# Kernel optimization log

Hardware: AMD Instinct MI355X
Metric: run time of the kernel (lower is better)

Reference implementation:

```python
import jax, jax.numpy as jnp
import numpy as np


def setup_inputs() -> dict:
    key = jax.random.key(0)
    k1, k2 = jax.random.split(key)
    B, L, D = 8, 4096, 64
    x = jax.random.normal(k1, (B, L, D), dtype=jnp.float32)
    # per-token validity mask [B, L, 1] with 0/1 entries (outer product builds the pairwise mask)
    mask = jax.random.randint(k2, (B, L, 1), 0, 2, dtype=jnp.int32)
    return {"x": x, "mask": mask}


def reference(x, mask):
    # OriAttention with head=1: q = k = v = x, shapes [B, L, D]
    B, L, D = x.shape
    scale = D ** 0.25  # note: fourth root of d, as in the original
    scores = jnp.einsum('bqd,bkd->bqk', x, x) / scale  # [B, L, L]
    # pairwise mask via outer product of the [B, L, 1] token mask, then bool cast
    mf = mask.astype(jnp.float32)
    pair = jnp.matmul(mf, mf.transpose(0, 2, 1)) != 0.0  # [B, L, L] bool
    scores = jnp.where(pair, scores, jnp.float32(-10000000.0))
    # original softmaxes along dim=2 of [B, H, Lq, Lk], i.e. over the QUERY axis
    attn = jax.nn.softmax(scores, axis=1)  # normalize over q for each k
    # then transposes (2,3) and matmuls with v: out[b,k,:] = sum_q attn[b,q,k] * v[b,q,:]
    out = jnp.einsum('bqk,bqd->bkd', attn, x)  # [B, L, D]
    return out
```

## Files before the change

### kernel.cpp

```cpp
#include <hip/hip_runtime.h>
#include <stdint.h>

typedef __attribute__((ext_vector_type(8))) __bf16 bf16x8;
typedef __attribute__((ext_vector_type(4))) __bf16 bf16x4;
typedef __attribute__((ext_vector_type(4))) float f32x4;

#define MFMA_BF16(A, B, C) __builtin_amdgcn_mfma_f32_16x16x32_bf16((A), (B), (C), 0, 0, 0)
#define VBAR() asm volatile("s_waitcnt vmcnt(0) lgkmcnt(0)\ns_barrier" ::: "memory")

__device__ __forceinline__ void gload16(const void* g, void* l) {
  __builtin_amdgcn_global_load_lds((const __attribute__((address_space(1))) void*)g,
                                   (__attribute__((address_space(3))) void*)l, 16, 0, 0);
}

namespace {

constexpr int kBatch = 8;
constexpr int kL = 4096;
constexpr int kD = 64;
constexpr int kQB = 128;
constexpr int kKB = 64;
constexpr int kSlotPad = 4096;
constexpr int kMaxTiles = 64;
constexpr int kSlotCap = 2304;
constexpr int kSplits = 8;
constexpr float kC = 1.4426950408889634f / 2.8284271247461903f;

constexpr size_t kWsPartialOff = 0;
constexpr size_t kWsCountOff = 65536;
constexpr size_t kWsRankOff = 131136;
constexpr size_t kWsPlOff = 196672;
constexpr size_t kWsXchOff = 1376320;
constexpr size_t kWsVtgOff = 5570624;
constexpr size_t kWsPaccOff = 9764928;

__device__ __forceinline__ int fk(int r) { return (r & 3) | ((r >> 1) & 4); }

__device__ __forceinline__ size_t slotrow(int s, int b, int slot, bool fb) {
  return fb ? ((size_t)b * kL + slot) : ((size_t)(s * kBatch + b) * kSlotCap + slot);
}

__global__ __launch_bounds__(256) void k_prep(const float* __restrict__ x,
                                              const int* __restrict__ mask,
                                              float* __restrict__ partial,
                                              uint16_t* __restrict__ rank,
                                              int* __restrict__ counts,
                                              __bf16* __restrict__ xch,
                                              __bf16* __restrict__ vtg) {
  const int b = blockIdx.y;
  const int bx = blockIdx.x;
  const int t = threadIdx.x;

  if (bx >= 64) {
    const int part = bx - 64;
    __shared__ float sm[256];
    const int d = t & 63, rs = t >> 6;
    const float* xb = x + (size_t)b * kL * kD;
    float s = 0.0f;
    const int r0 = part * 128 + rs;
    for (int i = 0; i < 32; ++i) s += xb[(size_t)(r0 + i * 4) * kD + d];
    sm[t] = s;
    __syncthreads();
    if (t < 64)
      partial[(b * 32 + part) * 64 + t] = sm[t] + sm[t + 64] + sm[t + 128] + sm[t + 192];
    return;
  }

  __shared__ int scan[256];
  __shared__ int slotTab[64];
  __shared__ __align__(16) __bf16 tmp[kKB][80];

  const int* mb = mask + b * kL;
  const int r0 = t * 16;
  int msk16 = 0, cnt = 0;
#pragma unroll
  for (int i = 0; i < 16; ++i) {
    if (mb[r0 + i] != 0) { msk16 |= 1 << i; ++cnt; }
  }
  scan[t] = cnt;
  if (t < 64) slotTab[t] = -1;
  __syncthreads();
#pragma unroll
  for (int off = 1; off < 256; off <<= 1) {
    const int v = (t >= off) ? scan[t - off] : 0;
    __syncthreads();
    scan[t] += v;
    __syncthreads();
  }
  const int count = scan[255];
  const int base = bx * 64;
  {
    int rk = scan[t] - cnt;
#pragma unroll
    for (int i = 0; i < 16; ++i) {
      if (msk16 & (1 << i)) {
        if (rk >= base && rk < base + 64) slotTab[rk - base] = r0 + i;
        ++rk;
      }
    }
  }
  if (bx == 0) {
    int rk = scan[t] - cnt;
#pragma unroll
    for (int i = 0; i < 16; ++i) {
      if (msk16 & (1 << i)) { rank[b * kL + r0 + i] = (uint16_t)rk; ++rk; }
    }
    if (t == 0) counts[b] = count;
  }
  __syncthreads();

  const int NT = (count + kKB - 1) >> 6;
  if (bx >= NT) return;

  const int srow = t >> 2, q3 = t & 3;
  const int slot = base + srow;
  const int rowi = slotTab[srow];
  float v16[16];
  if (rowi >= 0) {
    const float4* p = (const float4*)(x + ((size_t)b * kL + rowi) * kD + q3 * 16);
    const float4 a0 = p[0], a1 = p[1], a2 = p[2], a3 = p[3];
    v16[0] = a0.x; v16[1] = a0.y; v16[2] = a0.z; v16[3] = a0.w;
    v16[4] = a1.x; v16[5] = a1.y; v16[6] = a1.z; v16[7] = a1.w;
    v16[8] = a2.x; v16[9] = a2.y; v16[10] = a2.z; v16[11] = a2.w;
    v16[12] = a3.x; v16[13] = a3.y; v16[14] = a3.z; v16[15] = a3.w;
  } else {
#pragma unroll
    for (int i = 0; i < 16; ++i) v16[i] = 0.0f;
  }
  bf16x8 u0, u1;
#pragma unroll
  for (int j = 0; j < 8; ++j) { u0[j] = (__bf16)v16[j]; u1[j] = (__bf16)v16[8 + j]; }

  {
    __bf16* xrow = xch + ((size_t)b * kSlotPad + slot) * kD;
    const int f = fk(srow);
    *(bf16x8*)(xrow + (((2 * q3) ^ f) << 3)) = u0;
    *(bf16x8*)(xrow + (((2 * q3 + 1) ^ f) << 3)) = u1;
  }
  *(bf16x8*)&tmp[srow][q3 * 16] = u0;
  *(bf16x8*)&tmp[srow][q3 * 16 + 8] = u1;
  __syncthreads();
  {
    const int d = t >> 2, kq = t & 3;
    bf16x8 c0, c1;
#pragma unroll
    for (int i = 0; i < 8; ++i) {
      c0[i] = tmp[kq * 16 + i][d];
      c1[i] = tmp[kq * 16 + 8 + i][d];
    }
    __bf16* vrow = vtg + (((size_t)b * kMaxTiles + bx) * kKB + d) * kD;
    const int e = d & 7;
    *(bf16x8*)(vrow + (((2 * kq) ^ e) << 3)) = c0;
    *(bf16x8*)(vrow + (((2 * kq + 1) ^ e) << 3)) = c1;
  }
}

__global__ __launch_bounds__(256, 4) void k_attn(const __bf16* __restrict__ xch,
                                                 const __bf16* __restrict__ vtg,
                                                 const int* __restrict__ counts,
                                                 float* __restrict__ pl,
                                                 __bf16* __restrict__ pacc) {
  const int b = blockIdx.x;
  const int s = blockIdx.y;
  const int qt = blockIdx.z;

  int cmax = 0;
#pragma unroll
  for (int i = 0; i < kBatch; ++i) cmax = max(cmax, counts[i]);
  const bool fb = cmax > kSlotCap;
  const int nS = fb ? 1 : (int)gridDim.y;
  if (fb && s > 0) return;

  const int count = counts[b];
  if (qt * kQB >= count) return;
  const int NTtot = (count + kKB - 1) >> 6;
  const int TPS = (NTtot + nS - 1) / nS;
  const int t0 = s * TPS;
  const int t1 = min(NTtot, t0 + TPS);

  const int tid = threadIdx.x;
  const int wave = tid >> 6;
  const int lane = tid & 63;
  const int lg = lane >> 4;
  const int lr = lane & 15;

  int qpos[2];
  bool qvalid[2];
  size_t sr[2];
#pragma unroll
  for (int h = 0; h < 2; ++h) {
    qpos[h] = qt * kQB + h * 64 + wave * 16 + lr;
    qvalid[h] = qpos[h] < count;
    sr[h] = slotrow(s, b, qpos[h], fb);
  }

  if (t0 >= t1) {
#pragma unroll
    for (int h = 0; h < 2; ++h) {
      if (qvalid[h]) {
        const bf16x4 z = (bf16x4)(__bf16)0.0f;
#pragma unroll
        for (int dt = 0; dt < 4; ++dt) *(bf16x4*)&pacc[sr[h] * kD + dt * 16 + lg * 4] = z;
        if (lg == 0) pl[sr[h]] = 0.0f;
      }
    }
    return;
  }

  const __bf16* __restrict__ xb = xch + (size_t)b * kSlotPad * kD;
  const __bf16* __restrict__ vb = vtg + (size_t)b * kMaxTiles * (kKB * kD);

  __shared__ __align__(16) __bf16 KhB[2][kKB * kD];
  __shared__ __align__(16) __bf16 VtB[2][kKB * kD];

  bf16x8 qh[2][2];
#pragma unroll
  for (int h = 0; h < 2; ++h) {
    const int qr = qvalid[h] ? qpos[h] : 0;
    const __bf16* qrow = xb + (size_t)qr * kD;
    const int f = fk(qr & 63);
#pragma unroll
    for (int kt = 0; kt < 2; ++kt)
      qh[h][kt] = *(const bf16x8*)(qrow + (((kt * 4 + lg) ^ f) << 3));
  }

  f32x4 acc[2][4];
  f32x4 acc_l[2];
#pragma unroll
  for (int h = 0; h < 2; ++h) {
#pragma unroll
    for (int i = 0; i < 4; ++i) acc[h][i] = (f32x4)0.0f;
    acc_l[h] = (f32x4)0.0f;
  }

  bf16x8 vone;
#pragma unroll
  for (int j = 0; j < 8; ++j) vone[j] = (lr == 0) ? (__bf16)1.0f : (__bf16)0.0f;

  auto stage = [&](int t, int buf) {
    const size_t goff = (size_t)t * (kKB * kD);
    const int lo = lane * 8;
#pragma unroll
    for (int c = 0; c < 2; ++c) {
      const int eo = wave * 1024 + c * 512;
      gload16(xb + goff + eo + lo, &KhB[buf][eo]);
      gload16(vb + goff + eo + lo, &VtB[buf][eo]);
    }
  };

  stage(t0, 0);
  VBAR();

  int cur = 0;
  for (int t = t0; t < t1; ++t) {
    const bool havenext = (t + 1 < t1);
    if (havenext) stage(t + 1, cur ^ 1);

    const __bf16* Kh = &KhB[cur][0];
    const __bf16* Vt = &VtB[cur][0];

    f32x4 S_[2][2][2];
#pragma unroll
    for (int g = 0; g < 2; ++g) {
#pragma unroll
      for (int tt = 0; tt < 2; ++tt) {
        const int krow = g * 32 + ((lr >> 2) << 3) + tt * 4 + (lr & 3);
        const int f = fk(krow);
        f32x4 s0 = (f32x4)0.0f, s1 = (f32x4)0.0f;
#pragma unroll
        for (int kt = 0; kt < 2; ++kt) {
          const bf16x8 ah = *(const bf16x8*)&Kh[(krow << 6) + (((kt * 4 + lg) ^ f) << 3)];
          s0 = MFMA_BF16(ah, qh[0][kt], s0);
          s1 = MFMA_BF16(ah, qh[1][kt], s1);
        }
        S_[0][g][tt] = s0;
        S_[1][g][tt] = s1;
      }
    }

    float p[2][2][2][4];
#pragma unroll
    for (int h = 0; h < 2; ++h)
#pragma unroll
      for (int g = 0; g < 2; ++g)
#pragma unroll
        for (int tt = 0; tt < 2; ++tt)
#pragma unroll
          for (int r = 0; r < 4; ++r)
            p[h][g][tt][r] = __builtin_amdgcn_exp2f(S_[h][g][tt][r] * kC);

    if (t == NTtot - 1 && (count & 63)) {
      const int valid = count & 63;
#pragma unroll
      for (int h = 0; h < 2; ++h)
#pragma unroll
        for (int g = 0; g < 2; ++g)
#pragma unroll
          for (int tt = 0; tt < 2; ++tt)
#pragma unroll
            for (int r = 0; r < 4; ++r) {
              const int kl2 = g * 32 + lg * 8 + tt * 4 + r;
              if (kl2 >= valid) p[h][g][tt][r] = 0.0f;
            }
    }

    bf16x8 pf[2][2];
#pragma unroll
    for (int h = 0; h < 2; ++h)
#pragma unroll
      for (int g = 0; g < 2; ++g)
#pragma unroll
        for (int tt = 0; tt < 2; ++tt)
#pragma unroll
          for (int r = 0; r < 4; ++r) pf[h][g][tt * 4 + r] = (__bf16)p[h][g][tt][r];

#pragma unroll
    for (int g = 0; g < 2; ++g) {
      acc_l[0] = MFMA_BF16(vone, pf[0][g], acc_l[0]);
      acc_l[1] = MFMA_BF16(vone, pf[1][g], acc_l[1]);
#pragma unroll
      for (int dt = 0; dt < 4; ++dt) {
        const int d = dt * 16 + lr;
        const bf16x8 vf =
            *(const bf16x8*)&Vt[(d << 6) + ((((g << 2) + lg) ^ (d & 7)) << 3)];
        acc[0][dt] = MFMA_BF16(vf, pf[0][g], acc[0][dt]);
        acc[1][dt] = MFMA_BF16(vf, pf[1][g], acc[1][dt]);
      }
    }

    if (havenext) VBAR();
    cur ^= 1;
  }

#pragma unroll
  for (int h = 0; h < 2; ++h) {
    if (qvalid[h]) {
#pragma unroll
      for (int dt = 0; dt < 4; ++dt) {
        bf16x4 v;
#pragma unroll
        for (int r = 0; r < 4; ++r) v[r] = (__bf16)acc[h][dt][r];
        *(bf16x4*)&pacc[sr[h] * kD + dt * 16 + lg * 4] = v;
      }
      if (lg == 0) pl[sr[h]] = acc_l[h][0];
    }
  }
}

template <int TS>
__global__ __launch_bounds__(256) void k_post(const int* __restrict__ mask,
                                              const float* __restrict__ partial,
                                              const uint16_t* __restrict__ rank,
                                              const int* __restrict__ counts,
                                              const float* __restrict__ pl,
                                              const __bf16* __restrict__ pacc,
                                              float* __restrict__ out) {
  const int b = blockIdx.y;
  const int c = blockIdx.x;
  const int t = threadIdx.x;

  int cmax = 0;
#pragma unroll
  for (int i = 0; i < kBatch; ++i) cmax = max(cmax, counts[i]);
  const bool fb = cmax > kSlotCap;

  __shared__ float mean[64];
  __shared__ float winv[32];
  __shared__ int slotL[32];

  if (t < 64) {
    float s = 0.0f;
    for (int p = 0; p < 32; ++p) s += partial[(b * 32 + p) * 64 + t];
    mean[t] = s * (1.0f / (float)kL);
  } else if (t < 96) {
    const int i = t - 64;
    const int r = c * 32 + i;
    if (mask[b * kL + r] == 0) {
      slotL[i] = -1;
    } else {
      const int slot = rank[b * kL + r];
      slotL[i] = slot;
      float L = 0.0f;
      if (!fb) {
#pragma unroll
        for (int s2 = 0; s2 < TS; ++s2)
          L += pl[(size_t)(s2 * kBatch + b) * kSlotCap + slot];
      } else {
        L = pl[(size_t)b * kL + slot];
      }
      winv[i] = 1.0f / L;
    }
  }
  __syncthreads();

  const int d = t & 63;
#pragma unroll
  for (int it = 0; it < 8; ++it) {
    const int rl = it * 4 + (t >> 6);
    const int slot = slotL[rl];
    float o;
    if (slot < 0) {
      o = mean[d];
    } else if (!fb) {
      o = 0.0f;
#pragma unroll
      for (int s2 = 0; s2 < TS; ++s2)
        o += (float)pacc[((size_t)(s2 * kBatch + b) * kSlotCap + slot) * kD + d];
      o *= winv[rl];
    } else {
      o = winv[rl] * (float)pacc[((size_t)b * kL + slot) * kD + d];
    }
    out[((size_t)b * kL + c * 32 + rl) * kD + d] = o;
  }
}

}

extern "C" void kernel_launch(void* const* d_in, const int* in_sizes, int n_in,
                              void* d_out, int out_size, void* d_ws, size_t ws_size,
                              hipStream_t stream) {
  const float* x = (const float*)d_in[0];
  const int* mask = (const int*)d_in[1];
  float* out = (float*)d_out;
  char* ws = (char*)d_ws;
  float* partial = (float*)(ws + kWsPartialOff);
  int* counts = (int*)(ws + kWsCountOff);
  uint16_t* rank = (uint16_t*)(ws + kWsRankOff);
  float* pl = (float*)(ws + kWsPlOff);
  __bf16* xch = (__bf16*)(ws + kWsXchOff);
  __bf16* vtg = (__bf16*)(ws + kWsVtgOff);
  __bf16* pacc = (__bf16*)(ws + kWsPaccOff);

  int S = kSplits;
  while (S > 1 && ws_size < kWsPaccOff + (size_t)S * kBatch * kSlotCap * kD * 2) S >>= 1;

  k_prep<<<dim3(96, kBatch), dim3(256), 0, stream>>>(x, mask, partial, rank, counts,
                                                     xch, vtg);
  k_attn<<<dim3(kBatch, S, kL / kQB), dim3(256), 0, stream>>>(xch, vtg, counts, pl, pacc);
  switch (S) {
    case 8:
      k_post<8><<<dim3(128, kBatch), dim3(256), 0, stream>>>(mask, partial, rank, counts,
                                                             pl, pacc, out);
      break;
    case 4:
      k_post<4><<<dim3(128, kBatch), dim3(256), 0, stream>>>(mask, partial, rank, counts,
                                                             pl, pacc, out);
      break;
    case 2:
      k_post<2><<<dim3(128, kBatch), dim3(256), 0, stream>>>(mask, partial, rank, counts,
                                                             pl, pacc, out);
      break;
    default:
      k_post<1><<<dim3(128, kBatch), dim3(256), 0, stream>>>(mask, partial, rank, counts,
                                                             pl, pacc, out);
      break;
  }
}
```

Baseline: 40.31 us.

## Fuse split-K reduction and output scatter into attention kernel via last-block counter

Removes the separate post-processing kernel. Each attention block now publishes its partial accumulators with agent-scope atomic stores and bumps a per-(batch, query-tile) counter. The last-arriving split sums all partials, normalizes, and scatters rows to the output through a compacted index array. It also fills masked rows with the column mean. This saves a kernel launch and a pass over the partials, at the cost of an extra memset, atomics, and a serialized tail on the last block.

```diff
diff --git a/kernel.cpp b/kernel.cpp
--- a/kernel.cpp
+++ b/kernel.cpp
@@ -28,22 +28,27 @@
 
 constexpr size_t kWsPartialOff = 0;
 constexpr size_t kWsCountOff = 65536;
-constexpr size_t kWsRankOff = 131136;
+constexpr size_t kWsIdxOff = 131136;
 constexpr size_t kWsPlOff = 196672;
 constexpr size_t kWsXchOff = 1376320;
 constexpr size_t kWsVtgOff = 5570624;
 constexpr size_t kWsPaccOff = 9764928;
+constexpr size_t kWsQcntOff = 28639296;
 
 __device__ __forceinline__ int fk(int r) { return (r & 3) | ((r >> 1) & 4); }
 
 __device__ __forceinline__ size_t slotrow(int s, int b, int slot, bool fb) {
   return fb ? ((size_t)b * kL + slot) : ((size_t)(s * kBatch + b) * kSlotCap + slot);
+}
+
+__device__ __forceinline__ float bf16hi_f(uint32_t u) {
+  return __uint_as_float(u << 16);
 }
 
 __global__ __launch_bounds__(256) void k_prep(const float* __restrict__ x,
                                               const int* __restrict__ mask,
                                               float* __restrict__ partial,
-                                              uint16_t* __restrict__ rank,
+                                              uint16_t* __restrict__ idx,
                                               int* __restrict__ counts,
                                               __bf16* __restrict__ xch,
                                               __bf16* __restrict__ vtg) {
@@ -103,7 +108,7 @@
     int rk = scan[t] - cnt;
 #pragma unroll
     for (int i = 0; i < 16; ++i) {
-      if (msk16 & (1 << i)) { rank[b * kL + r0 + i] = (uint16_t)rk; ++rk; }
+      if (msk16 & (1 << i)) { idx[b * kL + rk] = (uint16_t)(r0 + i); ++rk; }
     }
     if (t == 0) counts[b] = count;
   }
@@ -155,11 +160,12 @@
   }
 }
 
-__global__ __launch_bounds__(256, 4) void k_attn(const __bf16* __restrict__ xch,
-                                                 const __bf16* __restrict__ vtg,
-                                                 const int* __restrict__ counts,
-                                                 float* __restrict__ pl,
-                                                 __bf16* __restrict__ pacc) {
+__global__ __launch_bounds__(256, 4) void k_attn(
+    const __bf16* __restrict__ xch, const __bf16* __restrict__ vtg,
+    const int* __restrict__ counts, float* __restrict__ pl,
+    __bf16* __restrict__ pacc, const uint16_t* __restrict__ idx,
+    const int* __restrict__ mask, const float* __restrict__ partial,
+    float* __restrict__ out, int* __restrict__ qcnt) {
   const int b = blockIdx.x;
   const int s = blockIdx.y;
   const int qt = blockIdx.z;
@@ -172,7 +178,7 @@
   if (fb && s > 0) return;
 
   const int count = counts[b];
-  if (qt * kQB >= count) return;
+  if (count > 0 && qt * kQB >= count) return;
   const int NTtot = (count + kKB - 1) >> 6;
   const int TPS = (NTtot + nS - 1) / nS;
   const int t0 = s * TPS;
@@ -184,6 +190,12 @@
   const int lg = lane >> 4;
   const int lr = lane & 15;
 
+  __shared__ __align__(16) __bf16 KhB[2][kKB * kD];
+  __shared__ __align__(16) __bf16 VtB[2][kKB * kD];
+  __shared__ float meanL[64];
+  __shared__ float linv[kQB];
+  __shared__ int lastF;
+
   int qpos[2];
   bool qvalid[2];
   size_t sr[2];
@@ -198,99 +210,86 @@
 #pragma unroll
     for (int h = 0; h < 2; ++h) {
       if (qvalid[h]) {
-        const bf16x4 z = (bf16x4)(__bf16)0.0f;
-#pragma unroll
-        for (int dt = 0; dt < 4; ++dt) *(bf16x4*)&pacc[sr[h] * kD + dt * 16 + lg * 4] = z;
-        if (lg == 0) pl[sr[h]] = 0.0f;
-      }
-    }
-    return;
-  }
-
-  const __bf16* __restrict__ xb = xch + (size_t)b * kSlotPad * kD;
-  const __bf16* __restrict__ vb = vtg + (size_t)b * kMaxTiles * (kKB * kD);
-
-  __shared__ __align__(16) __bf16 KhB[2][kKB * kD];
-  __shared__ __align__(16) __bf16 VtB[2][kKB * kD];
-
-  bf16x8 qh[2][2];
-#pragma unroll
-  for (int h = 0; h < 2; ++h) {
-    const int qr = qvalid[h] ? qpos[h] : 0;
-    const __bf16* qrow = xb + (size_t)qr * kD;
-    const int f = fk(qr & 63);
-#pragma unroll
-    for (int kt = 0; kt < 2; ++kt)
-      qh[h][kt] = *(const bf16x8*)(qrow + (((kt * 4 + lg) ^ f) << 3));
-  }
-
-  f32x4 acc[2][4];
-  f32x4 acc_l[2];
-#pragma unroll
-  for (int h = 0; h < 2; ++h) {
-#pragma unroll
-    for (int i = 0; i < 4; ++i) acc[h][i] = (f32x4)0.0f;
-    acc_l[h] = (f32x4)0.0f;
-  }
-
-  bf16x8 vone;
-#pragma unroll
-  for (int j = 0; j < 8; ++j) vone[j] = (lr == 0) ? (__bf16)1.0f : (__bf16)0.0f;
-
-  auto stage = [&](int t, int buf) {
-    const size_t goff = (size_t)t * (kKB * kD);
-    const int lo = lane * 8;
-#pragma unroll
-    for (int c = 0; c < 2; ++c) {
-      const int eo = wave * 1024 + c * 512;
-      gload16(xb + goff + eo + lo, &KhB[buf][eo]);
-      gload16(vb + goff + eo + lo, &VtB[buf][eo]);
-    }
-  };
-
-  stage(t0, 0);
-  VBAR();
-
-  int cur = 0;
-  for (int t = t0; t < t1; ++t) {
-    const bool havenext = (t + 1 < t1);
-    if (havenext) stage(t + 1, cur ^ 1);
-
-    const __bf16* Kh = &KhB[cur][0];
-    const __bf16* Vt = &VtB[cur][0];
-
-    f32x4 S_[2][2][2];
-#pragma unroll
-    for (int g = 0; g < 2; ++g) {
-#pragma unroll
-      for (int tt = 0; tt < 2; ++tt) {
-        const int krow = g * 32 + ((lr >> 2) << 3) + tt * 4 + (lr & 3);
-        const int f = fk(krow);
-        f32x4 s0 = (f32x4)0.0f, s1 = (f32x4)0.0f;
-#pragma unroll
-        for (int kt = 0; kt < 2; ++kt) {
-          const bf16x8 ah = *(const bf16x8*)&Kh[(krow << 6) + (((kt * 4 + lg) ^ f) << 3)];
-          s0 = MFMA_BF16(ah, qh[0][kt], s0);
-          s1 = MFMA_BF16(ah, qh[1][kt], s1);
+#pragma unroll
+        for (int dt = 0; dt < 4; ++dt)
+          __hip_atomic_store((unsigned long long*)&pacc[sr[h] * kD + dt * 16 + lg * 4],
+                             0ull, __ATOMIC_RELAXED, __HIP_MEMORY_SCOPE_AGENT);
+        if (lg == 0)
+          __hip_atomic_store(&pl[sr[h]], 0.0f, __ATOMIC_RELAXED,
+                             __HIP_MEMORY_SCOPE_AGENT);
+      }
+    }
+  } else {
+    const __bf16* __restrict__ xb = xch + (size_t)b * kSlotPad * kD;
+    const __bf16* __restrict__ vb = vtg + (size_t)b * kMaxTiles * (kKB * kD);
+
+    bf16x8 qh[2][2];
+#pragma unroll
+    for (int h = 0; h < 2; ++h) {
+      const int qr = qvalid[h] ? qpos[h] : 0;
+      const __bf16* qrow = xb + (size_t)qr * kD;
+      const int f = fk(qr & 63);
+#pragma unroll
+      for (int kt = 0; kt < 2; ++kt)
+        qh[h][kt] = *(const bf16x8*)(qrow + (((kt * 4 + lg) ^ f) << 3));
+    }
+
+    f32x4 acc[2][4];
+    f32x4 acc_l[2];
+#pragma unroll
+    for (int h = 0; h < 2; ++h) {
+#pragma unroll
+      for (int i = 0; i < 4; ++i) acc[h][i] = (f32x4)0.0f;
+      acc_l[h] = (f32x4)0.0f;
+    }
+
+    bf16x8 vone;
+#pragma unroll
+    for (int j = 0; j < 8; ++j) vone[j] = (lr == 0) ? (__bf16)1.0f : (__bf16)0.0f;
+
+    auto stage = [&](int t, int buf) {
+      const size_t goff = (size_t)t * (kKB * kD);
+      const int lo = lane * 8;
+#pragma unroll
+      for (int c = 0; c < 2; ++c) {
+        const int eo = wave * 1024 + c * 512;
+        gload16(xb + goff + eo + lo, &KhB[buf][eo]);
+        gload16(vb + goff + eo + lo, &VtB[buf][eo]);
+      }
+    };
+
+    stage(t0, 0);
+    VBAR();
+
+    int cur = 0;
+    for (int t = t0; t < t1; ++t) {
+      const bool havenext = (t + 1 < t1);
+      if (havenext) stage(t + 1, cur ^ 1);
+
+      const __bf16* Kh = &KhB[cur][0];
+      const __bf16* Vt = &VtB[cur][0];
+
+      f32x4 S_[2][2][2];
+#pragma unroll
+      for (int g = 0; g < 2; ++g) {
+#pragma unroll
+        for (int tt = 0; tt < 2; ++tt) {
+          const int krow = g * 32 + ((lr >> 2) << 3) + tt * 4 + (lr & 3);
+          const int f = fk(krow);
+          f32x4 s0 = (f32x4)0.0f, s1 = (f32x4)0.0f;
+#pragma unroll
+          for (int kt = 0; kt < 2; ++kt) {
+            const bf16x8 ah =
+                *(const bf16x8*)&Kh[(krow << 6) + (((kt * 4 + lg) ^ f) << 3)];
+            s0 = MFMA_BF16(ah, qh[0][kt], s0);
+            s1 = MFMA_BF16(ah, qh[1][kt], s1);
+          }
+          S_[0][g][tt] = s0;
+          S_[1][g][tt] = s1;
         }
-        S_[0][g][tt] = s0;
-        S_[1][g][tt] = s1;
-      }
-    }
-
-    float p[2][2][2][4];
-#pragma unroll
-    for (int h = 0; h < 2; ++h)
-#pragma unroll
-      for (int g = 0; g < 2; ++g)
-#pragma unroll
-        for (int tt = 0; tt < 2; ++tt)
-#pragma unroll
-          for (int r = 0; r < 4; ++r)
-            p[h][g][tt][r] = __builtin_amdgcn_exp2f(S_[h][g][tt][r] * kC);
-
-    if (t == NTtot - 1 && (count & 63)) {
-      const int valid = count & 63;
+      }
+
+      float p[2][2][2][4];
 #pragma unroll
       for (int h = 0; h < 2; ++h)
 #pragma unroll
@@ -298,119 +297,133 @@
 #pragma unroll
           for (int tt = 0; tt < 2; ++tt)
 #pragma unroll
-            for (int r = 0; r < 4; ++r) {
-              const int kl2 = g * 32 + lg * 8 + tt * 4 + r;
-              if (kl2 >= valid) p[h][g][tt][r] = 0.0f;
-            }
-    }
-
-    bf16x8 pf[2][2];
-#pragma unroll
-    for (int h = 0; h < 2; ++h)
-#pragma unroll
-      for (int g = 0; g < 2; ++g)
-#pragma unroll
-        for (int tt = 0; tt < 2; ++tt)
-#pragma unroll
-          for (int r = 0; r < 4; ++r) pf[h][g][tt * 4 + r] = (__bf16)p[h][g][tt][r];
-
-#pragma unroll
-    for (int g = 0; g < 2; ++g) {
-      acc_l[0] = MFMA_BF16(vone, pf[0][g], acc_l[0]);
-      acc_l[1] = MFMA_BF16(vone, pf[1][g], acc_l[1]);
-#pragma unroll
-      for (int dt = 0; dt < 4; ++dt) {
-        const int d = dt * 16 + lr;
-        const bf16x8 vf =
-            *(const bf16x8*)&Vt[(d << 6) + ((((g << 2) + lg) ^ (d & 7)) << 3)];
-        acc[0][dt] = MFMA_BF16(vf, pf[0][g], acc[0][dt]);
-        acc[1][dt] = MFMA_BF16(vf, pf[1][g], acc[1][dt]);
-      }
-    }
-
-    if (havenext) VBAR();
-    cur ^= 1;
-  }
-
-#pragma unroll
-  for (int h = 0; h < 2; ++h) {
-    if (qvalid[h]) {
-#pragma unroll
-      for (int dt = 0; dt < 4; ++dt) {
-        bf16x4 v;
-#pragma unroll
-        for (int r = 0; r < 4; ++r) v[r] = (__bf16)acc[h][dt][r];
-        *(bf16x4*)&pacc[sr[h] * kD + dt * 16 + lg * 4] = v;
-      }
-      if (lg == 0) pl[sr[h]] = acc_l[h][0];
-    }
-  }
-}
-
-template <int TS>
-__global__ __launch_bounds__(256) void k_post(const int* __restrict__ mask,
-                                              const float* __restrict__ partial,
-                                              const uint16_t* __restrict__ rank,
-                                              const int* __restrict__ counts,
-                                              const float* __restrict__ pl,
-                                              const __bf16* __restrict__ pacc,
-                                              float* __restrict__ out) {
-  const int b = blockIdx.y;
-  const int c = blockIdx.x;
-  const int t = threadIdx.x;
-
-  int cmax = 0;
-#pragma unroll
-  for (int i = 0; i < kBatch; ++i) cmax = max(cmax, counts[i]);
-  const bool fb = cmax > kSlotCap;
-
-  __shared__ float mean[64];
-  __shared__ float winv[32];
-  __shared__ int slotL[32];
-
-  if (t < 64) {
-    float s = 0.0f;
-    for (int p = 0; p < 32; ++p) s += partial[(b * 32 + p) * 64 + t];
-    mean[t] = s * (1.0f / (float)kL);
-  } else if (t < 96) {
-    const int i = t - 64;
-    const int r = c * 32 + i;
-    if (mask[b * kL + r] == 0) {
-      slotL[i] = -1;
-    } else {
-      const int slot = rank[b * kL + r];
-      slotL[i] = slot;
+            for (int r = 0; r < 4; ++r)
+              p[h][g][tt][r] = __builtin_amdgcn_exp2f(S_[h][g][tt][r] * kC);
+
+      if (t == NTtot - 1 && (count & 63)) {
+        const int valid = count & 63;
+#pragma unroll
+        for (int h = 0; h < 2; ++h)
+#pragma unroll
+          for (int g = 0; g < 2; ++g)
+#pragma unroll
+            for (int tt = 0; tt < 2; ++tt)
+#pragma unroll
+              for (int r = 0; r < 4; ++r) {
+                const int kl2 = g * 32 + lg * 8 + tt * 4 + r;
+                if (kl2 >= valid) p[h][g][tt][r] = 0.0f;
+              }
+      }
+
+      bf16x8 pf[2][2];
+#pragma unroll
+      for (int h = 0; h < 2; ++h)
+#pragma unroll
+        for (int g = 0; g < 2; ++g)
+#pragma unroll
+          for (int tt = 0; tt < 2; ++tt)
+#pragma unroll
+            for (int r = 0; r < 4; ++r) pf[h][g][tt * 4 + r] = (__bf16)p[h][g][tt][r];
+
+#pragma unroll
+      for (int g = 0; g < 2; ++g) {
+        acc_l[0] = MFMA_BF16(vone, pf[0][g], acc_l[0]);
+        acc_l[1] = MFMA_BF16(vone, pf[1][g], acc_l[1]);
+#pragma unroll
+        for (int dt = 0; dt < 4; ++dt) {
+          const int d = dt * 16 + lr;
+          const bf16x8 vf =
+              *(const bf16x8*)&Vt[(d << 6) + ((((g << 2) + lg) ^ (d & 7)) << 3)];
+          acc[0][dt] = MFMA_BF16(vf, pf[0][g], acc[0][dt]);
+          acc[1][dt] = MFMA_BF16(vf, pf[1][g], acc[1][dt]);
+        }
+      }
+
+      if (havenext) VBAR();
+      cur ^= 1;
+    }
+
+#pragma unroll
+    for (int h = 0; h < 2; ++h) {
+      if (qvalid[h]) {
+#pragma unroll
+        for (int dt = 0; dt < 4; ++dt) {
+          bf16x4 v;
+#pragma unroll
+          for (int r = 0; r < 4; ++r) v[r] = (__bf16)acc[h][dt][r];
+          unsigned long long uv;
+          __builtin_memcpy(&uv, &v, 8);
+          __hip_atomic_store((unsigned long long*)&pacc[sr[h] * kD + dt * 16 + lg * 4],
+                             uv, __ATOMIC_RELAXED, __HIP_MEMORY_SCOPE_AGENT);
+        }
+        if (lg == 0)
+          __hip_atomic_store(&pl[sr[h]], acc_l[h][0], __ATOMIC_RELAXED,
+                             __HIP_MEMORY_SCOPE_AGENT);
+      }
+    }
+  }
+
+  asm volatile("s_waitcnt vmcnt(0)" ::: "memory");
+  __syncthreads();
+  if (tid == 0) {
+    const int old = __hip_atomic_fetch_add(qcnt + (b * 32 + qt) * 16, 1,
+                                           __ATOMIC_RELAXED, __HIP_MEMORY_SCOPE_AGENT);
+    lastF = (old == nS - 1);
+  }
+  __syncthreads();
+  if (!lastF) return;
+
+  if (tid < 64) {
+    float sm = 0.0f;
+    for (int p2 = 0; p2 < 32; ++p2) sm += partial[(b * 32 + p2) * 64 + tid];
+    meanL[tid] = sm * (1.0f / (float)kL);
+  } else if (tid >= 128) {
+    const int sl = tid - 128;
+    const int slot = qt * kQB + sl;
+    if (slot < count) {
       float L = 0.0f;
-      if (!fb) {
-#pragma unroll
-        for (int s2 = 0; s2 < TS; ++s2)
-          L += pl[(size_t)(s2 * kBatch + b) * kSlotCap + slot];
-      } else {
-        L = pl[(size_t)b * kL + slot];
-      }
-      winv[i] = 1.0f / L;
-    }
-  }
-  __syncthreads();
-
-  const int d = t & 63;
-#pragma unroll
-  for (int it = 0; it < 8; ++it) {
-    const int rl = it * 4 + (t >> 6);
-    const int slot = slotL[rl];
-    float o;
-    if (slot < 0) {
-      o = mean[d];
-    } else if (!fb) {
-      o = 0.0f;
-#pragma unroll
-      for (int s2 = 0; s2 < TS; ++s2)
-        o += (float)pacc[((size_t)(s2 * kBatch + b) * kSlotCap + slot) * kD + d];
-      o *= winv[rl];
-    } else {
-      o = winv[rl] * (float)pacc[((size_t)b * kL + slot) * kD + d];
-    }
-    out[((size_t)b * kL + c * 32 + rl) * kD + d] = o;
+      for (int s2 = 0; s2 < nS; ++s2)
+        L += __hip_atomic_load(&pl[slotrow(s2, b, slot, fb)], __ATOMIC_RELAXED,
+                               __HIP_MEMORY_SCOPE_AGENT);
+      linv[sl] = 1.0f / L;
+    }
+  }
+  __syncthreads();
+
+  {
+    const int d0 = (tid & 31) * 2;
+    const int sg = tid >> 5;
+    const uint32_t* pacc32 = (const uint32_t*)pacc;
+    for (int i = 0; i < 16; ++i) {
+      const int sl = sg + i * 8;
+      const int slot = qt * kQB + sl;
+      if (slot < count) {
+        float o0 = 0.0f, o1 = 0.0f;
+        for (int s2 = 0; s2 < nS; ++s2) {
+          const size_t ro = slotrow(s2, b, slot, fb);
+          const uint32_t v = __hip_atomic_load(pacc32 + ro * 32 + (d0 >> 1),
+                                               __ATOMIC_RELAXED,
+                                               __HIP_MEMORY_SCOPE_AGENT);
+          o0 += bf16hi_f(v & 0xFFFFu);
+          o1 += bf16hi_f(v >> 16);
+        }
+        const float w = linv[sl];
+        const int row = idx[b * kL + slot];
+        float2 o = {o0 * w, o1 * w};
+        *(float2*)&out[((size_t)b * kL + row) * kD + d0] = o;
+      }
+    }
+  }
+
+  {
+    const int NQT = max(1, (count + kQB - 1) >> 7);
+    const int chunk = (kL + NQT - 1) / NQT;
+    const int rbeg = qt * chunk;
+    const int rend = min(kL, rbeg + chunk);
+    const int d = tid & 63;
+    for (int r = rbeg + (tid >> 6); r < rend; r += 4) {
+      if (mask[b * kL + r] == 0) out[((size_t)b * kL + r) * kD + d] = meanL[d];
+    }
   }
 }
 
@@ -425,34 +438,19 @@
   char* ws = (char*)d_ws;
   float* partial = (float*)(ws + kWsPartialOff);
   int* counts = (int*)(ws + kWsCountOff);
-  uint16_t* rank = (uint16_t*)(ws + kWsRankOff);
+  uint16_t* idx = (uint16_t*)(ws + kWsIdxOff);
   float* pl = (float*)(ws + kWsPlOff);
   __bf16* xch = (__bf16*)(ws + kWsXchOff);
   __bf16* vtg = (__bf16*)(ws + kWsVtgOff);
   __bf16* pacc = (__bf16*)(ws + kWsPaccOff);
+  int* qcnt = (int*)(ws + kWsQcntOff);
 
   int S = kSplits;
-  while (S > 1 && ws_size < kWsPaccOff + (size_t)S * kBatch * kSlotCap * kD * 2) S >>= 1;
-
-  k_prep<<<dim3(96, kBatch), dim3(256), 0, stream>>>(x, mask, partial, rank, counts,
+  while (S > 1 && ws_size < kWsQcntOff + 16384) S >>= 1;
+
+  hipMemsetAsync(ws + kWsQcntOff, 0, 16384, stream);
+  k_prep<<<dim3(96, kBatch), dim3(256), 0, stream>>>(x, mask, partial, idx, counts,
                                                      xch, vtg);
-  k_attn<<<dim3(kBatch, S, kL / kQB), dim3(256), 0, stream>>>(xch, vtg, counts, pl, pacc);
-  switch (S) {
-    case 8:
-      k_post<8><<<dim3(128, kBatch), dim3(256), 0, stream>>>(mask, partial, rank, counts,
-                                                             pl, pacc, out);
-      break;
-    case 4:
-      k_post<4><<<dim3(128, kBatch), dim3(256), 0, stream>>>(mask, partial, rank, counts,
-                                                             pl, pacc, out);
-      break;
-    case 2:
-      k_post<2><<<dim3(128, kBatch), dim3(256), 0, stream>>>(mask, partial, rank, counts,
-                                                             pl, pacc, out);
-      break;
-    default:
-      k_post<1><<<dim3(128, kBatch), dim3(256), 0, stream>>>(mask, partial, rank, counts,
-                                                             pl, pacc, out);
-      break;
-  }
-}
+  k_attn<<<dim3(kBatch, S, kL / kQB), dim3(256), 0, stream>>>(
+      xch, vtg, counts, pl, pacc, idx, mask, partial, out, qcnt);
+}
```

Result: slower. 91.77 us (+127.6%).
